# Optimization experiments

Measured on AMD Instinct MI355X. Metric: run time of the kernel, lower is better.

The kernel has to match this reference:

```python
import jax, jax.numpy as jnp
import numpy as np

TOP_K = 8
ROUTED_SCALING = 2.5


def setup_inputs() -> dict:
    key = jax.random.key(0)
    ks = jax.random.split(key, 8)
    B, S, H, E, I = 2, 1024, 2048, 32, 1024
    IS = 2 * I  # shared expert intermediate (n_shared_experts * moe_intermediate_size)
    w = lambda k, shape: jax.random.normal(k, shape, dtype=jnp.float32) * 0.02
    return {
        "hidden_states": jax.random.normal(ks[0], (B, S, H), dtype=jnp.float32),
        "gate_weight": w(ks[1], (E, H)),
        "w_gate": w(ks[2], (E, H, I)),
        "w_up": w(ks[3], (E, H, I)),
        "w_down": w(ks[4], (E, I, H)),
        "ws_gate": w(ks[5], (H, IS)),
        "ws_up": w(ks[6], (H, IS)),
        "ws_down": w(ks[7], (IS, H)),
    }


def reference(hidden_states, gate_weight, w_gate, w_up, w_down, ws_gate, ws_up, ws_down):
    B, S, H = hidden_states.shape
    x = hidden_states.reshape(-1, H)  # [T, H]
    T = x.shape[0]
    E = gate_weight.shape[0]

    # --- gate (DeepseekV3 top-k router: sigmoid scores, top-k, renormalize, scale) ---
    scores = jax.nn.sigmoid(x @ gate_weight.T)              # [T, E]
    topk_w, topk_i = jax.lax.top_k(scores, TOP_K)           # [T, K]
    topk_w = topk_w / (jnp.sum(topk_w, axis=-1, keepdims=True) + 1e-20)
    topk_w = topk_w * ROUTED_SCALING

    # dense [T, E] combine weights (scatter of top-k weights; zeros elsewhere)
    dense_w = jnp.zeros((T, E), dtype=topk_w.dtype).at[
        jnp.arange(T)[:, None], topk_i
    ].add(topk_w)

    # --- all experts on all tokens (calibrate_all_experts semantics; non-selected get weight 0) ---
    g = jnp.einsum('th,ehi->eti', x, w_gate)                # [E, T, I]
    u = jnp.einsum('th,ehi->eti', x, w_up)                  # [E, T, I]
    eo = jnp.einsum('eti,eih->eth', jax.nn.silu(g) * u, w_down)  # [E, T, H]
    routed = jnp.einsum('eth,te->th', eo, dense_w)          # weighted scatter-combine

    # --- shared expert (gated SiLU MLP on residual) ---
    shared = (jax.nn.silu(x @ ws_gate) * (x @ ws_up)) @ ws_down

    return (routed + shared).reshape(B, S, H)
```

## Files before the change

### kernel.cpp

```cpp
#include <hip/hip_runtime.h>

#define T_TOK 2048
#define H_DIM 2048
#define E_NUM 32
#define I_DIM 1024
#define IS_DIM 2048
#define K_TOT (E_NUM * I_DIM + IS_DIM)
#define SLOT_CAP 2048
#define NE_ALL 34
#define GU_TILES 192
#define DN_TILES 176
#define ACT_SLOTS 24576

typedef __bf16 bf16x8 __attribute__((ext_vector_type(8)));
typedef float  f32x4  __attribute__((ext_vector_type(4)));
static_assert(sizeof(bf16x8) == 16, "bf16x8 must be 16B");

#define OFF_CNT   ((size_t)0)
#define OFF_NTGU  ((size_t)192)
#define OFF_NTDN  ((size_t)196)
#define OFF_BASE  ((size_t)256)
#define OFF_TGU   ((size_t)512)
#define OFF_TDN   ((size_t)1280)
#define OFF_PAIRS ((size_t)2048)
#define OFF_XB    ((size_t)280576)
#define OFF_WGT   ((size_t)8669184)
#define OFF_WUT   ((size_t)142886912)
#define OFF_WSGT  ((size_t)277104640)
#define OFF_WSUT  ((size_t)285493248)
#define OFF_WDT   ((size_t)293881856)
#define OFF_ACT   ((size_t)436488192)

__device__ __forceinline__ unsigned short f2bf(float f) {
  unsigned int u = __float_as_uint(f);
  u += 0x7fffu + ((u >> 16) & 1u);
  return (unsigned short)(u >> 16);
}

__device__ __forceinline__ void gld16(const void* g, void* l) {
  __builtin_amdgcn_global_load_lds(
      (const __attribute__((address_space(1))) unsigned int*)g,
      (__attribute__((address_space(3))) unsigned int*)l, 16, 0, 0);
}

__global__ __launch_bounds__(256) void router_kernel(
    const float* __restrict__ x, const float* __restrict__ gw,
    int* __restrict__ cnt, unsigned int* __restrict__ pairs)
{
  const int t = blockIdx.x;
  __shared__ float xs[H_DIM];
  __shared__ float sc[E_NUM];
  const float4* xr = (const float4*)(x + (long)t * H_DIM);
  for (int i = threadIdx.x; i < H_DIM / 4; i += 256) ((float4*)xs)[i] = xr[i];
  __syncthreads();
  const int e = threadIdx.x >> 3, p = threadIdx.x & 7;
  const float4* ga = (const float4*)(gw + (long)e * H_DIM);
  const float4* xa = (const float4*)xs;
  float s = 0.f;
  #pragma unroll 4
  for (int i = p * 64; i < p * 64 + 64; ++i) {
    float4 a = ga[i], b = xa[i];
    s += a.x * b.x + a.y * b.y + a.z * b.z + a.w * b.w;
  }
  s += __shfl_down(s, 4, 8);
  s += __shfl_down(s, 2, 8);
  s += __shfl_down(s, 1, 8);
  if (p == 0) sc[e] = 1.f / (1.f + expf(-s));
  __syncthreads();
  if (threadIdx.x == 0) {
    float v[E_NUM];
    #pragma unroll
    for (int i = 0; i < E_NUM; ++i) v[i] = sc[i];
    unsigned mask = 0; float sum = 0.f;
    int sel[8]; float wv[8];
    for (int k = 0; k < 8; ++k) {
      float best = -1.f; int bi = 0;
      for (int i = 0; i < E_NUM; ++i)
        if (!((mask >> i) & 1u) && v[i] > best) { best = v[i]; bi = i; }
      mask |= 1u << bi; sel[k] = bi; wv[k] = best; sum += best;
    }
    const float scale = 2.5f / (sum + 1e-20f);
    for (int k = 0; k < 8; ++k) {
      const int slot = atomicAdd(&cnt[sel[k]], 1);
      if (slot < SLOT_CAP) {
        const unsigned int w16 = (unsigned int)f2bf(wv[k] * scale);
        pairs[sel[k] * SLOT_CAP + slot] = (w16 << 16) | (unsigned int)t;
      }
    }
  }
}

__global__ __launch_bounds__(256) void build_tiles_kernel(
    int* __restrict__ cnt, int* __restrict__ base,
    unsigned int* __restrict__ tgu, int* __restrict__ ntgu,
    unsigned int* __restrict__ tdn, int* __restrict__ ntdn,
    unsigned int* __restrict__ pairs)
{
  const int t = threadIdx.x;
  for (int s = t; s < T_TOK; s += 256) {
    const unsigned int pv = (0x3F80u << 16) | (unsigned int)s;
    pairs[32 * SLOT_CAP + s] = pv;
    pairs[33 * SLOT_CAP + s] = pv;
  }
  if (t == 0) {
    cnt[32] = T_TOK; cnt[33] = T_TOK;
    int b = 0, ngu = 0, ndn = 0;
    for (int e = 0; e < NE_ALL; ++e) {
      const int c = (e < 32) ? cnt[e] : T_TOK;
      base[e] = b;
      for (int m0 = 0; m0 < c; m0 += 128) {
        tgu[ngu++] = ((unsigned int)e << 16) | (unsigned int)m0;
        if (e < 33) tdn[ndn++] = ((unsigned int)e << 16) | (unsigned int)m0;
      }
      b += (c + 127) & ~127;
    }
    *ntgu = ngu; *ntdn = ndn;
  }
}

__global__ __launch_bounds__(256) void cvt_bf16_kernel(
    const float* __restrict__ in, unsigned short* __restrict__ out, int n4)
{
  int i = blockIdx.x * 256 + threadIdx.x;
  if (i >= n4) return;
  float4 v = ((const float4*)in)[i];
  ushort4 o;
  o.x = f2bf(v.x); o.y = f2bf(v.y); o.z = f2bf(v.z); o.w = f2bf(v.w);
  ((ushort4*)out)[i] = o;
}

struct TDescTable {
  const float* in[6];
  unsigned short* out[6];
  int C[6];
  int ldout[6];
  long in_bs[6];
  long out_bs[6];
  int nbx[6];
  int nbxy[6];
  int start[7];
};

__global__ __launch_bounds__(256) void transpose_fused(TDescTable td)
{
  const int bid = blockIdx.x;
  int i = 0;
  while (i < 5 && bid >= td.start[i + 1]) ++i;
  const int local = bid - td.start[i];
  const int bz = local / td.nbxy[i];
  const int rem = local % td.nbxy[i];
  const int by = rem / td.nbx[i];
  const int bx = rem % td.nbx[i];
  const float* in = td.in[i] + (long)bz * td.in_bs[i];
  unsigned short* out = td.out[i] + (long)bz * td.out_bs[i];
  const int C = td.C[i], ldout = td.ldout[i];

  __shared__ unsigned short tile[64][258];
  const int c0 = bx * 64;
  const int r0 = by * 256;
  const int t = threadIdx.x;
  const int rl0 = t >> 4;
  const int cl0 = (t & 15) * 4;

  float4 v[16];
  #pragma unroll
  for (int p = 0; p < 16; ++p) {
    const int rl = p * 16 + rl0;
    v[p] = *(const float4*)(in + (long)(r0 + rl) * C + c0 + cl0);
  }
  __builtin_amdgcn_sched_barrier(0);
  #pragma unroll
  for (int p = 0; p < 16; ++p) {
    const int rl = p * 16 + rl0;
    tile[cl0 + 0][rl] = f2bf(v[p].x);
    tile[cl0 + 1][rl] = f2bf(v[p].y);
    tile[cl0 + 2][rl] = f2bf(v[p].z);
    tile[cl0 + 3][rl] = f2bf(v[p].w);
  }
  __syncthreads();
  const int cw = t >> 5;
  const int rw = (t & 31) * 8;
  #pragma unroll
  for (int q = 0; q < 8; ++q) {
    const int cl = q * 8 + cw;
    const char* src = (const char*)&tile[cl][rw];
    uint4 o;
    o.x = *(const unsigned int*)(src + 0);
    o.y = *(const unsigned int*)(src + 4);
    o.z = *(const unsigned int*)(src + 8);
    o.w = *(const unsigned int*)(src + 12);
    *(uint4*)(out + (long)(c0 + cl) * ldout + r0 + rw) = o;
  }
}

__global__ __launch_bounds__(512, 4) void gate_up_moe_kernel(
    const unsigned short* __restrict__ xb,
    const unsigned short* __restrict__ bgT,
    const unsigned short* __restrict__ buT,
    const unsigned short* __restrict__ sgT,
    const unsigned short* __restrict__ suT,
    const int* __restrict__ cnt,
    const int* __restrict__ base,
    const unsigned int* __restrict__ pairs,
    const unsigned int* __restrict__ tiles,
    const int* __restrict__ ntp,
    unsigned short* __restrict__ act)
{
  const int ti = blockIdx.y;
  if (ti >= *ntp) return;
  const unsigned int tile = tiles[ti];
  const int e  = (int)(tile >> 16);
  const int m0 = (int)(tile & 0xFFFFu);
  const int cnte = cnt[e];
  const int be = base[e];
  const int n0 = blockIdx.x * 64;
  const long panel = (long)I_DIM * H_DIM;
  const unsigned short* Bg =
      ((e < 32) ? bgT + e * panel : sgT + (e - 32) * panel) + (long)n0 * H_DIM;
  const unsigned short* Bu =
      ((e < 32) ? buT + e * panel : suT + (e - 32) * panel) + (long)n0 * H_DIM;

  __shared__ unsigned short sA[2][128 * 64];
  __shared__ unsigned short sBg[2][64 * 64];
  __shared__ unsigned short sBu[2][64 * 64];

  const int tid = threadIdx.x;
  const int lane = tid & 63;
  const int wid = tid >> 6;
  const int wm = wid >> 1, wn = wid & 1;
  const int l15 = lane & 15;
  const int lk  = (lane >> 4) * 8;
  const int srow = tid >> 3;
  const int scol = (tid & 7) * 8;
  const int scolsw = (((tid & 7) ^ (srow & 7))) * 8;
  const int ksw = (l15 & 7) << 3;

  const unsigned short* asrc[2];
  #pragma unroll
  for (int r = 0; r < 2; ++r) {
    const int slot = m0 + r * 64 + srow;
    const unsigned int pr = (slot < cnte) ? pairs[e * SLOT_CAP + slot] : 0u;
    asrc[r] = xb + (long)(pr & 0xFFFFu) * H_DIM + scolsw;
  }

  const f32x4 fz = {0.f, 0.f, 0.f, 0.f};
  f32x4 accg[2][2], accu[2][2];
  #pragma unroll
  for (int i = 0; i < 2; ++i)
    #pragma unroll
    for (int j = 0; j < 2; ++j) { accg[i][j] = fz; accu[i][j] = fz; }

#define STAGE_GU(buf, k0) do {                                                 \
    gld16(asrc[0] + (k0), sA[buf] + srow * 64 + scol);                         \
    gld16(asrc[1] + (k0), sA[buf] + (64 + srow) * 64 + scol);                  \
    gld16(Bg + (long)srow * H_DIM + (k0) + scolsw,                             \
          sBg[buf] + srow * 64 + scol);                                        \
    gld16(Bu + (long)srow * H_DIM + (k0) + scolsw,                             \
          sBu[buf] + srow * 64 + scol);                                        \
  } while (0)

#define COMP_GU(buf) do {                                                      \
    __builtin_amdgcn_s_setprio(1);                                             \
    _Pragma("unroll")                                                          \
    for (int kk = 0; kk < 2; ++kk) {                                           \
      const int ko = kk * 32 + lk;                                             \
      bf16x8 a[2], g[2], u[2];                                                 \
      _Pragma("unroll")                                                        \
      for (int mi = 0; mi < 2; ++mi)                                           \
        a[mi] = *(const bf16x8*)(sA[buf] + (wm * 32 + mi * 16 + l15) * 64 +    \
                                 (ko ^ ksw));                                  \
      _Pragma("unroll")                                                        \
      for (int ni = 0; ni < 2; ++ni) {                                         \
        g[ni] = *(const bf16x8*)(sBg[buf] + (wn * 32 + ni * 16 + l15) * 64 +   \
                                 (ko ^ ksw));                                  \
        u[ni] = *(const bf16x8*)(sBu[buf] + (wn * 32 + ni * 16 + l15) * 64 +   \
                                 (ko ^ ksw));                                  \
      }                                                                        \
      _Pragma("unroll")                                                        \
      for (int mi = 0; mi < 2; ++mi)                                           \
        _Pragma("unroll")                                                      \
        for (int ni = 0; ni < 2; ++ni) {                                       \
          accg[mi][ni] = __builtin_amdgcn_mfma_f32_16x16x32_bf16(              \
              a[mi], g[ni], accg[mi][ni], 0, 0, 0);                            \
          accu[mi][ni] = __builtin_amdgcn_mfma_f32_16x16x32_bf16(              \
              a[mi], u[ni], accu[mi][ni], 0, 0, 0);                            \
        }                                                                      \
    }                                                                          \
    __builtin_amdgcn_s_setprio(0);                                             \
  } while (0)

  STAGE_GU(0, 0);
  __syncthreads();
  for (int t = 0; t < 32; t += 2) {
    if (t + 1 < 32) STAGE_GU(1, (t + 1) * 64);
    COMP_GU(0);
    __syncthreads();
    if (t + 2 < 32) STAGE_GU(0, (t + 2) * 64);
    COMP_GU(1);
    __syncthreads();
  }
#undef STAGE_GU
#undef COMP_GU

  const int colb = n0 + wn * 32;
  #pragma unroll
  for (int mi = 0; mi < 2; ++mi) {
    #pragma unroll
    for (int r = 0; r < 4; ++r) {
      const int slot = m0 + wm * 32 + mi * 16 + (lane >> 4) * 4 + r;
      if (slot < cnte) {
        const unsigned int pr = pairs[e * SLOT_CAP + slot];
        const float w = __uint_as_float(pr & 0xFFFF0000u);
        #pragma unroll
        for (int ni = 0; ni < 2; ++ni) {
          const float gv = accg[mi][ni][r];
          const float uv = accu[mi][ni][r];
          const float sv = (gv / (1.f + expf(-gv))) * uv * w;
          act[((long)(be + slot)) * I_DIM + colb + ni * 16 + l15] = f2bf(sv);
        }
      }
    }
  }
}

__global__ __launch_bounds__(512, 4) void down_moe_kernel(
    const unsigned short* __restrict__ act,
    const unsigned short* __restrict__ wdT,
    const int* __restrict__ cnt,
    const int* __restrict__ base,
    const unsigned int* __restrict__ pairs,
    const unsigned int* __restrict__ tiles,
    const int* __restrict__ ntp,
    float* __restrict__ out)
{
  const int ti = blockIdx.y;
  if (ti >= *ntp) return;
  const unsigned int tile = tiles[ti];
  const int e  = (int)(tile >> 16);
  const int m0 = (int)(tile & 0xFFFFu);
  const int cnte = cnt[e];
  const int n0 = blockIdx.x * 64;
  const unsigned short* A = act + ((long)base[e] + m0) * I_DIM;
  const unsigned short* B = wdT + (long)n0 * K_TOT + (long)e * I_DIM;
  const int nk = (e == 32) ? 32 : 16;

  __shared__ unsigned short sA[2][128 * 64];
  __shared__ unsigned short sB[2][64 * 64];

  const int tid = threadIdx.x;
  const int lane = tid & 63;
  const int wid = tid >> 6;
  const int wm = wid >> 1, wn = wid & 1;
  const int l15 = lane & 15;
  const int lk  = (lane >> 4) * 8;
  const int srow = tid >> 3;
  const int scol = (tid & 7) * 8;
  const int scolsw = (((tid & 7) ^ (srow & 7))) * 8;
  const int ksw = (l15 & 7) << 3;

  const f32x4 fz = {0.f, 0.f, 0.f, 0.f};
  f32x4 acc[2][2];
  #pragma unroll
  for (int i = 0; i < 2; ++i)
    #pragma unroll
    for (int j = 0; j < 2; ++j) acc[i][j] = fz;

#define STAGE_DN(buf, k0) do {                                                 \
    const long koff = (long)((k0) & 1023) +                                    \
                      (long)((k0) >> 10) * (2048L * 1024L);                    \
    gld16(A + (long)srow * I_DIM + koff + scolsw,                              \
          sA[buf] + srow * 64 + scol);                                         \
    gld16(A + (long)(64 + srow) * I_DIM + koff + scolsw,                       \
          sA[buf] + (64 + srow) * 64 + scol);                                  \
    gld16(B + (long)srow * K_TOT + (k0) + scolsw,                              \
          sB[buf] + srow * 64 + scol);                                         \
  } while (0)

#define COMP_DN(buf) do {                                                      \
    __builtin_amdgcn_s_setprio(1);                                             \
    _Pragma("unroll")                                                          \
    for (int kk = 0; kk < 2; ++kk) {                                           \
      const int ko = kk * 32 + lk;                                             \
      bf16x8 a[2], b[2];                                                       \
      _Pragma("unroll")                                                        \
      for (int mi = 0; mi < 2; ++mi)                                           \
        a[mi] = *(const bf16x8*)(sA[buf] + (wm * 32 + mi * 16 + l15) * 64 +    \
                                 (ko ^ ksw));                                  \
      _Pragma("unroll")                                                        \
      for (int ni = 0; ni < 2; ++ni)                                           \
        b[ni] = *(const bf16x8*)(sB[buf] + (wn * 32 + ni * 16 + l15) * 64 +    \
                                 (ko ^ ksw));                                  \
      _Pragma("unroll")                                                        \
      for (int mi = 0; mi < 2; ++mi)                                           \
        _Pragma("unroll")                                                      \
        for (int ni = 0; ni < 2; ++ni)                                         \
          acc[mi][ni] = __builtin_amdgcn_mfma_f32_16x16x32_bf16(               \
              a[mi], b[ni], acc[mi][ni], 0, 0, 0);                             \
    }                                                                          \
    __builtin_amdgcn_s_setprio(0);                                             \
  } while (0)

  STAGE_DN(0, 0);
  __syncthreads();
  for (int t = 0; t < 32; t += 2) {
    if (t >= nk) break;
    if (t + 1 < nk) STAGE_DN(1, (t + 1) * 64);
    COMP_DN(0);
    __syncthreads();
    if (t + 2 < nk) STAGE_DN(0, (t + 2) * 64);
    COMP_DN(1);
    __syncthreads();
  }
#undef STAGE_DN
#undef COMP_DN

  #pragma unroll
  for (int mi = 0; mi < 2; ++mi) {
    #pragma unroll
    for (int r = 0; r < 4; ++r) {
      const int slot = m0 + wm * 32 + mi * 16 + (lane >> 4) * 4 + r;
      if (slot < cnte) {
        const int tok = (int)(pairs[e * SLOT_CAP + slot] & 0xFFFFu);
        #pragma unroll
        for (int ni = 0; ni < 2; ++ni)
          atomicAdd(out + (long)tok * H_DIM + n0 + wn * 32 + ni * 16 + l15,
                    acc[mi][ni][r]);
      }
    }
  }
}

extern "C" void kernel_launch(void* const* d_in, const int* in_sizes, int n_in,
                              void* d_out, int out_size, void* d_ws, size_t ws_size,
                              hipStream_t stream) {
  (void)in_sizes; (void)n_in; (void)ws_size;
  const float* x   = (const float*)d_in[0];
  const float* gw  = (const float*)d_in[1];
  const float* wg  = (const float*)d_in[2];
  const float* wu  = (const float*)d_in[3];
  const float* wd  = (const float*)d_in[4];
  const float* wsg = (const float*)d_in[5];
  const float* wsu = (const float*)d_in[6];
  const float* wsd = (const float*)d_in[7];
  float* out = (float*)d_out;
  char* ws = (char*)d_ws;

  int*            cnt   = (int*)(ws + OFF_CNT);
  int*            ntgu  = (int*)(ws + OFF_NTGU);
  int*            ntdn  = (int*)(ws + OFF_NTDN);
  int*            basep = (int*)(ws + OFF_BASE);
  unsigned int*   tgu   = (unsigned int*)(ws + OFF_TGU);
  unsigned int*   tdn   = (unsigned int*)(ws + OFF_TDN);
  unsigned int*   pairs = (unsigned int*)(ws + OFF_PAIRS);
  unsigned short* xb    = (unsigned short*)(ws + OFF_XB);
  unsigned short* wgT   = (unsigned short*)(ws + OFF_WGT);
  unsigned short* wuT   = (unsigned short*)(ws + OFF_WUT);
  unsigned short* wsgT  = (unsigned short*)(ws + OFF_WSGT);
  unsigned short* wsuT  = (unsigned short*)(ws + OFF_WSUT);
  unsigned short* wdT   = (unsigned short*)(ws + OFF_WDT);
  unsigned short* actb  = (unsigned short*)(ws + OFF_ACT);

  hipMemsetAsync(ws + OFF_CNT, 0, 256, stream);
  hipMemsetAsync(out, 0, (size_t)out_size * sizeof(float), stream);

  router_kernel<<<T_TOK, 256, 0, stream>>>(x, gw, cnt, pairs);
  build_tiles_kernel<<<1, 256, 0, stream>>>(cnt, basep, tgu, ntgu, tdn, ntdn,
                                            pairs);
  cvt_bf16_kernel<<<(T_TOK * H_DIM / 4 + 255) / 256, 256, 0, stream>>>(
      x, xb, T_TOK * H_DIM / 4);

  TDescTable td;
  td.in[0] = wg;  td.out[0] = wgT;  td.C[0] = I_DIM;  td.ldout[0] = H_DIM;
  td.in_bs[0] = (long)H_DIM * I_DIM; td.out_bs[0] = (long)I_DIM * H_DIM;
  td.nbx[0] = I_DIM / 64; td.nbxy[0] = (I_DIM / 64) * (H_DIM / 256);
  td.in[1] = wu;  td.out[1] = wuT;  td.C[1] = I_DIM;  td.ldout[1] = H_DIM;
  td.in_bs[1] = (long)H_DIM * I_DIM; td.out_bs[1] = (long)I_DIM * H_DIM;
  td.nbx[1] = I_DIM / 64; td.nbxy[1] = (I_DIM / 64) * (H_DIM / 256);
  td.in[2] = wd;  td.out[2] = wdT;  td.C[2] = H_DIM;  td.ldout[2] = K_TOT;
  td.in_bs[2] = (long)I_DIM * H_DIM; td.out_bs[2] = (long)I_DIM;
  td.nbx[2] = H_DIM / 64; td.nbxy[2] = (H_DIM / 64) * (I_DIM / 256);
  td.in[3] = wsg; td.out[3] = wsgT; td.C[3] = IS_DIM; td.ldout[3] = H_DIM;
  td.in_bs[3] = 0; td.out_bs[3] = 0;
  td.nbx[3] = IS_DIM / 64; td.nbxy[3] = (IS_DIM / 64) * (H_DIM / 256);
  td.in[4] = wsu; td.out[4] = wsuT; td.C[4] = IS_DIM; td.ldout[4] = H_DIM;
  td.in_bs[4] = 0; td.out_bs[4] = 0;
  td.nbx[4] = IS_DIM / 64; td.nbxy[4] = (IS_DIM / 64) * (H_DIM / 256);
  td.in[5] = wsd; td.out[5] = wdT + E_NUM * I_DIM; td.C[5] = H_DIM;
  td.ldout[5] = K_TOT; td.in_bs[5] = 0; td.out_bs[5] = 0;
  td.nbx[5] = H_DIM / 64; td.nbxy[5] = (H_DIM / 64) * (IS_DIM / 256);
  td.start[0] = 0;
  for (int i = 0; i < 5; ++i) {
    int nz = (i <= 2) ? E_NUM : 1;
    td.start[i + 1] = td.start[i] + td.nbxy[i] * nz;
  }
  td.start[6] = td.start[5] + td.nbxy[5];
  transpose_fused<<<td.start[6], 256, 0, stream>>>(td);

  gate_up_moe_kernel<<<dim3(16, GU_TILES), 512, 0, stream>>>(
      xb, wgT, wuT, wsgT, wsuT, cnt, basep, pairs, tgu, ntgu, actb);

  down_moe_kernel<<<dim3(32, DN_TILES), 512, 0, stream>>>(
      actb, wdT, cnt, basep, pairs, tdn, ntdn, out);
}
```

Before: 845.2 us.

## Enlarge per-warp MFMA tiles with 256-thread blocks, dropping double buffering

Both MoE GEMM kernels go from 512 to 256 threads per block, and each warp now computes a larger output tile (64 rows, with 64 columns in the down kernel). The down kernel's block tile grows to 128x128, which halves the grid along N. LDS double buffering is replaced by a single-buffer load, sync, compute, sync loop. The aim is more MFMA work per shared-memory fragment load and less redundant staging, at the cost of higher register pressure and no overlap between global loads and compute.

```diff
diff --git a/kernel.cpp b/kernel.cpp
--- a/kernel.cpp
+++ b/kernel.cpp
@@ -193,7 +193,7 @@
   }
 }
 
-__global__ __launch_bounds__(512, 4) void gate_up_moe_kernel(
+__global__ __launch_bounds__(256) void gate_up_moe_kernel(
     const unsigned short* __restrict__ xb,
     const unsigned short* __restrict__ bgT,
     const unsigned short* __restrict__ buT,
@@ -220,9 +220,9 @@
   const unsigned short* Bu =
       ((e < 32) ? buT + e * panel : suT + (e - 32) * panel) + (long)n0 * H_DIM;
 
-  __shared__ unsigned short sA[2][128 * 64];
-  __shared__ unsigned short sBg[2][64 * 64];
-  __shared__ unsigned short sBu[2][64 * 64];
+  __shared__ unsigned short sA[128 * 64];
+  __shared__ unsigned short sBg[64 * 64];
+  __shared__ unsigned short sBu[64 * 64];
 
   const int tid = threadIdx.x;
   const int lane = tid & 63;
@@ -235,79 +235,64 @@
   const int scolsw = (((tid & 7) ^ (srow & 7))) * 8;
   const int ksw = (l15 & 7) << 3;
 
-  const unsigned short* asrc[2];
-  #pragma unroll
-  for (int r = 0; r < 2; ++r) {
-    const int slot = m0 + r * 64 + srow;
+  const unsigned short* asrc[4];
+  #pragma unroll
+  for (int r = 0; r < 4; ++r) {
+    const int slot = m0 + r * 32 + srow;
     const unsigned int pr = (slot < cnte) ? pairs[e * SLOT_CAP + slot] : 0u;
     asrc[r] = xb + (long)(pr & 0xFFFFu) * H_DIM + scolsw;
   }
 
   const f32x4 fz = {0.f, 0.f, 0.f, 0.f};
-  f32x4 accg[2][2], accu[2][2];
-  #pragma unroll
-  for (int i = 0; i < 2; ++i)
+  f32x4 accg[4][2], accu[4][2];
+  #pragma unroll
+  for (int i = 0; i < 4; ++i)
     #pragma unroll
     for (int j = 0; j < 2; ++j) { accg[i][j] = fz; accu[i][j] = fz; }
 
-#define STAGE_GU(buf, k0) do {                                                 \
-    gld16(asrc[0] + (k0), sA[buf] + srow * 64 + scol);                         \
-    gld16(asrc[1] + (k0), sA[buf] + (64 + srow) * 64 + scol);                  \
-    gld16(Bg + (long)srow * H_DIM + (k0) + scolsw,                             \
-          sBg[buf] + srow * 64 + scol);                                        \
-    gld16(Bu + (long)srow * H_DIM + (k0) + scolsw,                             \
-          sBu[buf] + srow * 64 + scol);                                        \
-  } while (0)
-
-#define COMP_GU(buf) do {                                                      \
-    __builtin_amdgcn_s_setprio(1);                                             \
-    _Pragma("unroll")                                                          \
-    for (int kk = 0; kk < 2; ++kk) {                                           \
-      const int ko = kk * 32 + lk;                                             \
-      bf16x8 a[2], g[2], u[2];                                                 \
-      _Pragma("unroll")                                                        \
-      for (int mi = 0; mi < 2; ++mi)                                           \
-        a[mi] = *(const bf16x8*)(sA[buf] + (wm * 32 + mi * 16 + l15) * 64 +    \
-                                 (ko ^ ksw));                                  \
-      _Pragma("unroll")                                                        \
-      for (int ni = 0; ni < 2; ++ni) {                                         \
-        g[ni] = *(const bf16x8*)(sBg[buf] + (wn * 32 + ni * 16 + l15) * 64 +   \
-                                 (ko ^ ksw));                                  \
-        u[ni] = *(const bf16x8*)(sBu[buf] + (wn * 32 + ni * 16 + l15) * 64 +   \
-                                 (ko ^ ksw));                                  \
-      }                                                                        \
-      _Pragma("unroll")                                                        \
-      for (int mi = 0; mi < 2; ++mi)                                           \
-        _Pragma("unroll")                                                      \
-        for (int ni = 0; ni < 2; ++ni) {                                       \
-          accg[mi][ni] = __builtin_amdgcn_mfma_f32_16x16x32_bf16(              \
-              a[mi], g[ni], accg[mi][ni], 0, 0, 0);                            \
-          accu[mi][ni] = __builtin_amdgcn_mfma_f32_16x16x32_bf16(              \
-              a[mi], u[ni], accu[mi][ni], 0, 0, 0);                            \
-        }                                                                      \
-    }                                                                          \
-    __builtin_amdgcn_s_setprio(0);                                             \
-  } while (0)
-
-  STAGE_GU(0, 0);
-  __syncthreads();
-  for (int t = 0; t < 32; t += 2) {
-    if (t + 1 < 32) STAGE_GU(1, (t + 1) * 64);
-    COMP_GU(0);
+  for (int k0 = 0; k0 < H_DIM; k0 += 64) {
+    #pragma unroll
+    for (int r = 0; r < 4; ++r)
+      gld16(asrc[r] + k0, sA + (r * 32 + srow) * 64 + scol);
+    #pragma unroll
+    for (int r = 0; r < 2; ++r) {
+      gld16(Bg + (long)(r * 32 + srow) * H_DIM + k0 + scolsw,
+            sBg + (r * 32 + srow) * 64 + scol);
+      gld16(Bu + (long)(r * 32 + srow) * H_DIM + k0 + scolsw,
+            sBu + (r * 32 + srow) * 64 + scol);
+    }
     __syncthreads();
-    if (t + 2 < 32) STAGE_GU(0, (t + 2) * 64);
-    COMP_GU(1);
+    __builtin_amdgcn_s_setprio(1);
+    #pragma unroll
+    for (int kk = 0; kk < 2; ++kk) {
+      const int ko = kk * 32 + lk;
+      bf16x8 a[4], g[2], u[2];
+      #pragma unroll
+      for (int mi = 0; mi < 4; ++mi)
+        a[mi] = *(const bf16x8*)(sA + (wm * 64 + mi * 16 + l15) * 64 + (ko ^ ksw));
+      #pragma unroll
+      for (int ni = 0; ni < 2; ++ni) {
+        g[ni] = *(const bf16x8*)(sBg + (wn * 32 + ni * 16 + l15) * 64 + (ko ^ ksw));
+        u[ni] = *(const bf16x8*)(sBu + (wn * 32 + ni * 16 + l15) * 64 + (ko ^ ksw));
+      }
+      #pragma unroll
+      for (int mi = 0; mi < 4; ++mi)
+        #pragma unroll
+        for (int ni = 0; ni < 2; ++ni) {
+          accg[mi][ni] = __builtin_amdgcn_mfma_f32_16x16x32_bf16(a[mi], g[ni], accg[mi][ni], 0, 0, 0);
+          accu[mi][ni] = __builtin_amdgcn_mfma_f32_16x16x32_bf16(a[mi], u[ni], accu[mi][ni], 0, 0, 0);
+        }
+    }
+    __builtin_amdgcn_s_setprio(0);
     __syncthreads();
   }
-#undef STAGE_GU
-#undef COMP_GU
 
   const int colb = n0 + wn * 32;
   #pragma unroll
-  for (int mi = 0; mi < 2; ++mi) {
+  for (int mi = 0; mi < 4; ++mi) {
     #pragma unroll
     for (int r = 0; r < 4; ++r) {
-      const int slot = m0 + wm * 32 + mi * 16 + (lane >> 4) * 4 + r;
+      const int slot = m0 + wm * 64 + mi * 16 + (lane >> 4) * 4 + r;
       if (slot < cnte) {
         const unsigned int pr = pairs[e * SLOT_CAP + slot];
         const float w = __uint_as_float(pr & 0xFFFF0000u);
@@ -323,7 +308,7 @@
   }
 }
 
-__global__ __launch_bounds__(512, 4) void down_moe_kernel(
+__global__ __launch_bounds__(256) void down_moe_kernel(
     const unsigned short* __restrict__ act,
     const unsigned short* __restrict__ wdT,
     const int* __restrict__ cnt,
@@ -339,13 +324,13 @@
   const int e  = (int)(tile >> 16);
   const int m0 = (int)(tile & 0xFFFFu);
   const int cnte = cnt[e];
-  const int n0 = blockIdx.x * 64;
+  const int n0 = blockIdx.x * 128;
   const unsigned short* A = act + ((long)base[e] + m0) * I_DIM;
   const unsigned short* B = wdT + (long)n0 * K_TOT + (long)e * I_DIM;
   const int nk = (e == 32) ? 32 : 16;
 
-  __shared__ unsigned short sA[2][128 * 64];
-  __shared__ unsigned short sB[2][64 * 64];
+  __shared__ unsigned short sA[128 * 64];
+  __shared__ unsigned short sB[128 * 64];
 
   const int tid = threadIdx.x;
   const int lane = tid & 63;
@@ -359,71 +344,55 @@
   const int ksw = (l15 & 7) << 3;
 
   const f32x4 fz = {0.f, 0.f, 0.f, 0.f};
-  f32x4 acc[2][2];
-  #pragma unroll
-  for (int i = 0; i < 2; ++i)
-    #pragma unroll
-    for (int j = 0; j < 2; ++j) acc[i][j] = fz;
-
-#define STAGE_DN(buf, k0) do {                                                 \
-    const long koff = (long)((k0) & 1023) +                                    \
-                      (long)((k0) >> 10) * (2048L * 1024L);                    \
-    gld16(A + (long)srow * I_DIM + koff + scolsw,                              \
-          sA[buf] + srow * 64 + scol);                                         \
-    gld16(A + (long)(64 + srow) * I_DIM + koff + scolsw,                       \
-          sA[buf] + (64 + srow) * 64 + scol);                                  \
-    gld16(B + (long)srow * K_TOT + (k0) + scolsw,                              \
-          sB[buf] + srow * 64 + scol);                                         \
-  } while (0)
-
-#define COMP_DN(buf) do {                                                      \
-    __builtin_amdgcn_s_setprio(1);                                             \
-    _Pragma("unroll")                                                          \
-    for (int kk = 0; kk < 2; ++kk) {                                           \
-      const int ko = kk * 32 + lk;                                             \
-      bf16x8 a[2], b[2];                                                       \
-      _Pragma("unroll")                                                        \
-      for (int mi = 0; mi < 2; ++mi)                                           \
-        a[mi] = *(const bf16x8*)(sA[buf] + (wm * 32 + mi * 16 + l15) * 64 +    \
-                                 (ko ^ ksw));                                  \
-      _Pragma("unroll")                                                        \
-      for (int ni = 0; ni < 2; ++ni)                                           \
-        b[ni] = *(const bf16x8*)(sB[buf] + (wn * 32 + ni * 16 + l15) * 64 +    \
-                                 (ko ^ ksw));                                  \
-      _Pragma("unroll")                                                        \
-      for (int mi = 0; mi < 2; ++mi)                                           \
-        _Pragma("unroll")                                                      \
-        for (int ni = 0; ni < 2; ++ni)                                         \
-          acc[mi][ni] = __builtin_amdgcn_mfma_f32_16x16x32_bf16(               \
-              a[mi], b[ni], acc[mi][ni], 0, 0, 0);                             \
-    }                                                                          \
-    __builtin_amdgcn_s_setprio(0);                                             \
-  } while (0)
-
-  STAGE_DN(0, 0);
-  __syncthreads();
-  for (int t = 0; t < 32; t += 2) {
-    if (t >= nk) break;
-    if (t + 1 < nk) STAGE_DN(1, (t + 1) * 64);
-    COMP_DN(0);
+  f32x4 acc[4][4];
+  #pragma unroll
+  for (int i = 0; i < 4; ++i)
+    #pragma unroll
+    for (int j = 0; j < 4; ++j) acc[i][j] = fz;
+
+  for (int t = 0; t < nk; ++t) {
+    const int k0 = t * 64;
+    const long koff = (long)(k0 & 1023) + (long)(k0 >> 10) * (2048L * 1024L);
+    #pragma unroll
+    for (int r = 0; r < 4; ++r)
+      gld16(A + (long)(r * 32 + srow) * I_DIM + koff + scolsw,
+            sA + (r * 32 + srow) * 64 + scol);
+    #pragma unroll
+    for (int r = 0; r < 4; ++r)
+      gld16(B + (long)(r * 32 + srow) * K_TOT + k0 + scolsw,
+            sB + (r * 32 + srow) * 64 + scol);
     __syncthreads();
-    if (t + 2 < nk) STAGE_DN(0, (t + 2) * 64);
-    COMP_DN(1);
+    __builtin_amdgcn_s_setprio(1);
+    #pragma unroll
+    for (int kk = 0; kk < 2; ++kk) {
+      const int ko = kk * 32 + lk;
+      bf16x8 a[4], b[4];
+      #pragma unroll
+      for (int mi = 0; mi < 4; ++mi)
+        a[mi] = *(const bf16x8*)(sA + (wm * 64 + mi * 16 + l15) * 64 + (ko ^ ksw));
+      #pragma unroll
+      for (int ni = 0; ni < 4; ++ni)
+        b[ni] = *(const bf16x8*)(sB + (wn * 64 + ni * 16 + l15) * 64 + (ko ^ ksw));
+      #pragma unroll
+      for (int mi = 0; mi < 4; ++mi)
+        #pragma unroll
+        for (int ni = 0; ni < 4; ++ni)
+          acc[mi][ni] = __builtin_amdgcn_mfma_f32_16x16x32_bf16(a[mi], b[ni], acc[mi][ni], 0, 0, 0);
+    }
+    __builtin_amdgcn_s_setprio(0);
     __syncthreads();
   }
-#undef STAGE_DN
-#undef COMP_DN
-
-  #pragma unroll
-  for (int mi = 0; mi < 2; ++mi) {
+
+  #pragma unroll
+  for (int mi = 0; mi < 4; ++mi) {
     #pragma unroll
     for (int r = 0; r < 4; ++r) {
-      const int slot = m0 + wm * 32 + mi * 16 + (lane >> 4) * 4 + r;
+      const int slot = m0 + wm * 64 + mi * 16 + (lane >> 4) * 4 + r;
       if (slot < cnte) {
         const int tok = (int)(pairs[e * SLOT_CAP + slot] & 0xFFFFu);
         #pragma unroll
-        for (int ni = 0; ni < 2; ++ni)
-          atomicAdd(out + (long)tok * H_DIM + n0 + wn * 32 + ni * 16 + l15,
+        for (int ni = 0; ni < 4; ++ni)
+          atomicAdd(out + (long)tok * H_DIM + n0 + wn * 64 + ni * 16 + l15,
                     acc[mi][ni][r]);
       }
     }
@@ -496,9 +465,9 @@
   td.start[6] = td.start[5] + td.nbxy[5];
   transpose_fused<<<td.start[6], 256, 0, stream>>>(td);
 
-  gate_up_moe_kernel<<<dim3(16, GU_TILES), 512, 0, stream>>>(
+  gate_up_moe_kernel<<<dim3(16, GU_TILES), 256, 0, stream>>>(
       xb, wgT, wuT, wsgT, wsuT, cnt, basep, pairs, tgu, ntgu, actb);
 
-  down_moe_kernel<<<dim3(32, DN_TILES), 512, 0, stream>>>(
+  down_moe_kernel<<<dim3(16, DN_TILES), 256, 0, stream>>>(
       actb, wdT, cnt, basep, pairs, tdn, ntdn, out);
 }
```

After: 837.0 us. No clear change (-1.0%).
